# Kernel optimization log

Measured on AMD Instinct MI355X. Metric: run time of the kernel, lower is better.

Reference implementation:

```python
import jax, jax.numpy as jnp
import numpy as np

T, B, I, H = 512, 64, 512, 1024


def setup_inputs() -> dict:
    key = jax.random.key(0)
    ks = jax.random.split(key, 7)
    s = 0.03  # keep recurrent dynamics stable
    return {
        "X": jax.random.normal(ks[0], (T, B, I), jnp.float32),
        "h0": jax.random.normal(ks[1], (B, H), jnp.float32) * 0.1,
        "c0": jax.random.normal(ks[2], (B, H), jnp.float32) * 0.1,
        "Wi": jax.random.normal(ks[3], (4, I, H), jnp.float32) * s,
        "Wh": jax.random.normal(ks[4], (4, H, H), jnp.float32) * s,
        "bi": jnp.zeros((4, H), jnp.float32),
        "bh": jnp.zeros((4, H), jnp.float32),
    }


def reference(X, h0, c0, Wi, Wh, bi, bh):
    # Gate order along axis 0 of Wi/Wh/bi/bh: f, i, g, o (matches the torch module's
    # linear_if/hf, linear_ii/hi, linear_ig/hg, linear_io/ho pairs).
    b = bi + bh  # [4, H] combined bias, mathematically identical

    def step(carry, x_t):
        h, c = carry
        # z: [4, B, H] = x @ Wi_g + h @ Wh_g + b_g for each gate g
        z = (jnp.einsum('bi,gih->gbh', x_t, Wi)
             + jnp.einsum('bh,ghk->gbk', h, Wh)
             + b[:, None, :])
        f = jax.nn.sigmoid(z[0])
        i = jax.nn.sigmoid(z[1])
        g = jnp.tanh(z[2])
        o = jax.nn.sigmoid(z[3])
        c_new = f * c + i * g
        h_new = o * jnp.tanh(c_new)
        return (h_new, c_new), h_new

    (h_n, c_n), outputs = jax.lax.scan(step, (h0, c0), X)
    return outputs, h_n, c_n
```

## Files before the change

### kernel.cpp

```cpp
#include <hip/hip_runtime.h>
#include <stdint.h>

#define T_STEPS 512
#define NB 64
#define NI 512
#define NH 1024
#define NBLK 128

typedef __attribute__((ext_vector_type(8))) short short8;
typedef __attribute__((ext_vector_type(4))) float floatx4;
typedef __attribute__((ext_vector_type(16))) float floatx16;
typedef __attribute__((ext_vector_type(4))) unsigned short ushortx4;

__device__ __forceinline__ unsigned short f2bf(float f) {
  union { float f; uint32_t u; } v; v.f = f;
  return (unsigned short)((v.u + 0x7FFFu + ((v.u >> 16) & 1u)) >> 16);
}
__device__ __forceinline__ float bf2f(unsigned short s) {
  union { uint32_t u; float f; } v; v.u = ((uint32_t)s) << 16; return v.f;
}
__device__ __forceinline__ float sigmoid_f(float x) {
  return 1.0f / (1.0f + __expf(-x));
}
__device__ __forceinline__ float tanh_f(float x) {
  float xx = fminf(fmaxf(x, -15.0f), 15.0f);
  float e = __expf(2.0f * xx);
  return (e - 1.0f) / (e + 1.0f);
}


__global__ void convert_x(const float* __restrict__ X, unsigned short* __restrict__ Xb) {
  int i = blockIdx.x * 256 + threadIdx.x;
  floatx4 x = ((const floatx4*)X)[i];
  ushortx4 o;
  o[0] = f2bf(x[0]); o[1] = f2bf(x[1]); o[2] = f2bf(x[2]); o[3] = f2bf(x[3]);
  ((ushortx4*)Xb)[i] = o;
}

__global__ void transpose_bf16(const float* __restrict__ in, unsigned short* __restrict__ outp,
                               int K, int N) {
  __shared__ float tile[64][65];
  int g = blockIdx.z;
  int k0 = blockIdx.x * 64, n0 = blockIdx.y * 64;
  int tx = threadIdx.x & 63, ty = threadIdx.x >> 6;
  const float* src = in + (size_t)g * K * N;
  unsigned short* dst = outp + (size_t)g * K * N;
#pragma unroll
  for (int i = 0; i < 16; i++) {
    int r = ty * 16 + i;
    tile[r][tx] = src[(size_t)(k0 + r) * N + n0 + tx];
  }
  __syncthreads();
#pragma unroll
  for (int i = 0; i < 16; i++) {
    int r = ty * 16 + i;
    dst[(size_t)(n0 + r) * K + k0 + tx] = f2bf(tile[tx][r]);
  }
}

__global__ void prep_small(const float* __restrict__ bi, const float* __restrict__ bh,
                           const float* __restrict__ h0, float* __restrict__ bias,
                           unsigned short* __restrict__ hbuf0, unsigned* __restrict__ flags) {
  int i = blockIdx.x * 256 + threadIdx.x;
  if (i < NBLK) flags[i] = 0u;
  if (i < 4 * NH) bias[i] = bi[i] + bh[i];
  if (i < NB * NH) hbuf0[i] = f2bf(h0[i]);
}

__global__ __launch_bounds__(256) void gemm_zx(
    const unsigned short* __restrict__ Xb,
    const unsigned short* __restrict__ WibT,
    const float* __restrict__ bias,
    unsigned short* __restrict__ Zx) {
  __shared__ __align__(16) unsigned short As[128][40];
  __shared__ __align__(16) unsigned short Bs[128][40];
  const int g = blockIdx.z;
  const int m0 = blockIdx.x * 128;
  const int n0 = blockIdx.y * 128;
  const int tid = threadIdx.x;
  const int lane = tid & 63;
  const int wave = tid >> 6;
  const int wm = wave & 1, wn = wave >> 1;
  const int fr = lane & 15;
  const int fq = (lane >> 4) * 8;

  const unsigned short* Bsrc = WibT + (size_t)g * NH * NI;

  floatx4 acc[4][4];
#pragma unroll
  for (int a = 0; a < 4; a++)
#pragma unroll
    for (int b = 0; b < 4; b++)
#pragma unroll
      for (int z = 0; z < 4; z++) acc[a][b][z] = 0.0f;

  for (int k0 = 0; k0 < NI; k0 += 32) {
#pragma unroll
    for (int it = 0; it < 2; it++) {
      int c = tid + it * 256;
      int row = c >> 2, kc = (c & 3) * 8;
      *(uint4*)(&As[row][kc]) = *(const uint4*)(Xb + (size_t)(m0 + row) * NI + k0 + kc);
      *(uint4*)(&Bs[row][kc]) = *(const uint4*)(Bsrc + (size_t)(n0 + row) * NI + k0 + kc);
    }
    __syncthreads();
    short8 af[4], bf[4];
#pragma unroll
    for (int ms = 0; ms < 4; ms++) af[ms] = *(const short8*)(&As[wm * 64 + ms * 16 + fr][fq]);
#pragma unroll
    for (int ns = 0; ns < 4; ns++) bf[ns] = *(const short8*)(&Bs[wn * 64 + ns * 16 + fr][fq]);
#pragma unroll
    for (int ms = 0; ms < 4; ms++)
#pragma unroll
      for (int ns = 0; ns < 4; ns++)
        acc[ms][ns] = __builtin_amdgcn_mfma_f32_16x16x32_bf16(af[ms], bf[ns], acc[ms][ns], 0, 0, 0);
    __syncthreads();
  }

#pragma unroll
  for (int ns = 0; ns < 4; ns++) {
    int col = n0 + wn * 64 + ns * 16 + fr;
    float bs = bias[g * NH + col];
#pragma unroll
    for (int ms = 0; ms < 4; ms++) {
#pragma unroll
      for (int r = 0; r < 4; r++) {
        int m = m0 + wm * 64 + ms * 16 + (lane >> 4) * 4 + r;
        Zx[(size_t)m * 4096 + (size_t)g * NH + col] = f2bf(acc[ms][ns][r] + bs);
      }
    }
  }
}

__device__ __forceinline__ void issue_none() {}

template<int G>
__device__ __forceinline__ void load_a(const unsigned short* ap, short8 (&areg)[64]) {
  asm volatile("global_load_dwordx4 %0, %1, off offset:%2 sc0 sc1"
               : "=v"(areg[G]) : "v"(ap), "i"(G * 32));
}

template<int G>
__device__ __forceinline__ void load_b(const unsigned short* bfr, int lane, short8 (&bs)[64]) {
  bs[G] = *(const short8*)(&bfr[((size_t)(G * 64) + lane) * 8]);
}

template<int G>
struct Prolog {
  static __device__ __forceinline__ void run(const unsigned short* ap, short8 (&areg)[64]) {
    load_a<G>(ap, areg);
    Prolog<G + 1>::run(ap, areg);
  }
};
template<>
struct Prolog<16> {
  static __device__ __forceinline__ void run(const unsigned short*, short8 (&)[64]) {}
};

template<int G>
struct Chunks {
  static __device__ __forceinline__ void run(const unsigned short* ap, const unsigned short* bfr,
                                             int lane, short8 (&areg)[64], short8 (&bs)[64],
                                             floatx16& acc0, floatx16& acc1) {
    if constexpr (G + 16 < 64) load_a<G + 16>(ap, areg);
    if constexpr (G + 4 < 64) load_b<G + 4>(bfr, lane, bs);
    constexpr int NOUT = (G + 16 < 64) ? 16 : (63 - G);
    asm volatile("s_waitcnt vmcnt(%1)" : "+v"(areg[G]) : "i"(NOUT) : "memory");
    if constexpr ((G & 1) == 0)
      acc0 = __builtin_amdgcn_mfma_f32_32x32x16_bf16(areg[G], bs[G], acc0, 0, 0, 0);
    else
      acc1 = __builtin_amdgcn_mfma_f32_32x32x16_bf16(areg[G], bs[G], acc1, 0, 0, 0);
    Chunks<G + 1>::run(ap, bfr, lane, areg, bs, acc0, acc1);
  }
};
template<>
struct Chunks<64> {
  static __device__ __forceinline__ void run(const unsigned short*, const unsigned short*,
                                             int, short8 (&)[64], short8 (&)[64],
                                             floatx16&, floatx16&) {}
};

__global__ __launch_bounds__(128, 1) void lstm_persist(
    const unsigned short* __restrict__ Zx,
    const unsigned short* __restrict__ WhT,
    const float* __restrict__ c0,
    unsigned short* __restrict__ hbuf,
    unsigned* __restrict__ flags,
    float* __restrict__ out) {
  __shared__ __align__(16) unsigned short bfr[64 * 64 * 8];

  const int bk = blockIdx.x;
  const int j0 = bk * 8;
  const int tid = threadIdx.x;
  const int lane = tid & 63;
  const int wm = tid >> 6;
  const int nl = lane & 31;
  const int g0 = nl >> 3;
  const int jj = nl & 7;
  const int half = lane >> 5;

  for (int i = 0; i < 32; i++) {
    int f = tid + i * 128;
    int fl = f & 63, kk = f >> 6;
    int n = fl & 31;
    size_t wrow = (size_t)((n >> 3) * NH + j0 + (n & 7));
    int kb = kk * 16 + (fl >> 5) * 8;
    uint4 v = *(const uint4*)(WhT + wrow * NH + kb);
    *(uint4*)(&bfr[(size_t)f * 8]) = v;
  }

  float creg[16];
  int brow[16];
#pragma unroll
  for (int r = 0; r < 16; r++) {
    brow[r] = wm * 32 + (r & 3) + 8 * (r >> 2) + 4 * half;
    creg[r] = c0[(size_t)brow[r] * NH + j0 + jj];
  }
  __syncthreads();

  const int hsz = NB * NH;

  float zx[16];
  {
    const unsigned short* zbase = Zx + (size_t)g0 * NH + j0 + jj;
#pragma unroll
    for (int r = 0; r < 16; r++) zx[r] = bf2f(zbase[(size_t)brow[r] * 4096]);
  }

  for (int t = 0; t < T_STEPS; t++) {
    if (t) {
      unsigned tgt = (unsigned)t;
      for (;;) {
        unsigned a = __hip_atomic_load(flags + 2 * lane, __ATOMIC_RELAXED,
                                       __HIP_MEMORY_SCOPE_AGENT);
        unsigned b = __hip_atomic_load(flags + 2 * lane + 1, __ATOMIC_RELAXED,
                                       __HIP_MEMORY_SCOPE_AGENT);
        if (__all((int)(a >= tgt && b >= tgt))) break;
        __builtin_amdgcn_s_sleep(1);
      }
    }
    asm volatile("s_waitcnt vmcnt(0)" ::: "memory");
    __builtin_amdgcn_sched_barrier(0);

    const unsigned short* hin = hbuf + (size_t)(t & 1) * hsz;
    unsigned short* hout = hbuf + (size_t)((t + 1) & 1) * hsz;
    const unsigned short* ap = hin + (size_t)(wm * 32 + nl) * NH + half * 8;

    floatx16 acc0, acc1;
#pragma unroll
    for (int z = 0; z < 16; z++) { acc0[z] = 0.0f; acc1[z] = 0.0f; }

    short8 areg[64];
    short8 bs[64];
    Prolog<0>::run(ap, areg);
    load_b<0>(bfr, lane, bs);
    load_b<1>(bfr, lane, bs);
    load_b<2>(bfr, lane, bs);
    load_b<3>(bfr, lane, bs);
    Chunks<0>::run(ap, bfr, lane, areg, bs, acc0, acc1);
    __builtin_amdgcn_sched_barrier(0);

#pragma unroll
    for (int z = 0; z < 16; z++) acc0[z] += acc1[z];

#pragma unroll
    for (int r = 0; r < 16; r++) {
      float z0 = acc0[r] + zx[r];
      float z1 = __shfl_xor(z0, 8);
      float z2 = __shfl_xor(z0, 16);
      float z3 = __shfl_xor(z1, 16);
      bool bb0 = (g0 & 1) != 0, bb1 = (g0 & 2) != 0;
      float zf = bb1 ? (bb0 ? z3 : z2) : (bb0 ? z1 : z0);
      float zi = bb1 ? (bb0 ? z2 : z3) : (bb0 ? z0 : z1);
      float zg = bb1 ? (bb0 ? z1 : z0) : (bb0 ? z3 : z2);
      float zo = bb1 ? (bb0 ? z0 : z1) : (bb0 ? z2 : z3);
      float fg = sigmoid_f(zf);
      float ig = sigmoid_f(zi);
      float gg = tanh_f(zg);
      float og = sigmoid_f(zo);
      float c = fg * creg[r] + ig * gg;
      creg[r] = c;
      float h = og * tanh_f(c);
      if (g0 == 0) {
        size_t oidx = (size_t)brow[r] * NH + j0 + jj;
        out[(size_t)t * hsz + oidx] = h;
        __hip_atomic_store(&hout[oidx], f2bf(h), __ATOMIC_RELAXED,
                           __HIP_MEMORY_SCOPE_AGENT);
        if (t == T_STEPS - 1) out[(size_t)T_STEPS * hsz + oidx] = h;
      }
    }

    if (t + 1 < T_STEPS) {
      asm volatile("s_waitcnt vmcnt(0)" ::: "memory");
      __syncthreads();
      if (tid == 0)
        __hip_atomic_store(flags + bk, (unsigned)(t + 1),
                           __ATOMIC_RELAXED, __HIP_MEMORY_SCOPE_AGENT);
      const unsigned short* zbase =
          Zx + (size_t)(t + 1) * (NB * 4096) + (size_t)g0 * NH + j0 + jj;
#pragma unroll
      for (int r = 0; r < 16; r++) zx[r] = bf2f(zbase[(size_t)brow[r] * 4096]);
    }
  }

  if (g0 == 0) {
#pragma unroll
    for (int r = 0; r < 16; r++)
      out[(size_t)T_STEPS * NB * NH + NB * NH + (size_t)brow[r] * NH + j0 + jj] = creg[r];
  }
}

extern "C" void kernel_launch(void* const* d_in, const int* in_sizes, int n_in,
                              void* d_out, int out_size, void* d_ws, size_t ws_size,
                              hipStream_t stream) {
  const float* X  = (const float*)d_in[0];
  const float* h0 = (const float*)d_in[1];
  const float* c0 = (const float*)d_in[2];
  const float* Wi = (const float*)d_in[3];
  const float* Wh = (const float*)d_in[4];
  const float* bi = (const float*)d_in[5];
  const float* bh = (const float*)d_in[6];
  float* out = (float*)d_out;

  uint8_t* ws = (uint8_t*)d_ws;
  size_t off = 0;
  auto alloc = [&](size_t bytes) -> void* {
    void* p = ws + off;
    off += (bytes + 255) & ~(size_t)255;
    return p;
  };
  unsigned short* Zx   = (unsigned short*)alloc((size_t)T_STEPS * NB * 4096 * 2);
  unsigned short* Xb   = (unsigned short*)alloc((size_t)T_STEPS * NB * NI * 2);
  unsigned short* WibT = (unsigned short*)alloc((size_t)4 * NH * NI * 2);
  unsigned short* WhT  = (unsigned short*)alloc((size_t)4 * NH * NH * 2);
  float* bias          = (float*)alloc((size_t)4 * NH * 4);
  unsigned short* hbuf = (unsigned short*)alloc((size_t)2 * NB * NH * 2);
  unsigned* flags      = (unsigned*)alloc((size_t)NBLK * 32 * 4);

  if (off > ws_size) {
    hipMemsetAsync(d_out, 0x7F, (size_t)out_size * 4, stream);
    return;
  }

  convert_x<<<16384, 256, 0, stream>>>(X, Xb);
  transpose_bf16<<<dim3(8, 16, 4), 256, 0, stream>>>(Wi, WibT, NI, NH);
  transpose_bf16<<<dim3(16, 16, 4), 256, 0, stream>>>(Wh, WhT, NH, NH);
  prep_small<<<256, 256, 0, stream>>>(bi, bh, h0, bias, hbuf, flags);
  gemm_zx<<<dim3(256, 8, 4), 256, 0, stream>>>(Xb, WibT, bias, Zx);

  lstm_persist<<<dim3(NBLK), dim3(128), 0, stream>>>(Zx, WhT, c0, hbuf, flags, out);
}
```

Before: 5.807 ms.

## Repack Zx into per-block contiguous layout and prefetch it across the step

The input-projection GEMM now writes its bf16 results, staged through shared memory, in a layout where each persistent block's per-step gate slice is contiguous. The recurrent kernel can then fetch its 16 Zx values with two 16-byte non-temporal loads, issued right after the MFMA chain and double-buffered across a two-step unrolled loop, where it previously used 16 scattered scalar loads after the flag publish. The flag poll becomes one 64-bit load instead of two 32-bit loads, and the h output stores are moved after the flag release and made non-temporal, taking them off the critical path. The risks are extra shared memory in the GEMM, higher register pressure from the prefetch buffers, and a more complex index mapping.

Measured after the change: 6.048 ms. 4.1% more time.

```diff
diff --git a/kernel.cpp b/kernel.cpp
--- a/kernel.cpp
+++ b/kernel.cpp
@@ -71,9 +71,10 @@
     const unsigned short* __restrict__ Xb,
     const unsigned short* __restrict__ WibT,
     const float* __restrict__ bias,
-    unsigned short* __restrict__ Zx) {
+    unsigned short* __restrict__ Zq) {
   __shared__ __align__(16) unsigned short As[128][40];
   __shared__ __align__(16) unsigned short Bs[128][40];
+  __shared__ __align__(16) unsigned short stg[16384];
   const int g = blockIdx.z;
   const int m0 = blockIdx.x * 128;
   const int n0 = blockIdx.y * 128;
@@ -118,20 +119,37 @@
 
 #pragma unroll
   for (int ns = 0; ns < 4; ns++) {
-    int col = n0 + wn * 64 + ns * 16 + fr;
-    float bs = bias[g * NH + col];
+    int jrel = wn * 64 + ns * 16 + fr;
+    float bs = bias[g * NH + n0 + jrel];
+    int bkp = jrel >> 3, jj = jrel & 7;
 #pragma unroll
     for (int ms = 0; ms < 4; ms++) {
 #pragma unroll
       for (int r = 0; r < 4; r++) {
-        int m = m0 + wm * 64 + ms * 16 + (lane >> 4) * 4 + r;
-        Zx[(size_t)m * 4096 + (size_t)g * NH + col] = f2bf(acc[ms][ns][r] + bs);
+        int mrel = wm * 64 + ms * 16 + (lane >> 4) * 4 + r;
+        int tp = mrel >> 6, b = mrel & 63;
+        int wm2 = b >> 5, row32 = b & 31;
+        int half2 = (row32 >> 2) & 1;
+        int rr = (row32 & 3) | ((row32 >> 3) << 2);
+        int idx = (((((tp * 16 + bkp) * 2 + wm2) * 2 + half2) * 8 + jj) * 16) + rr;
+        stg[idx] = f2bf(acc[ms][ns][r] + bs);
       }
     }
   }
-}
-
-__device__ __forceinline__ void issue_none() {}
+  __syncthreads();
+  const size_t t0 = (size_t)(m0 >> 6);
+  const int bk0 = n0 >> 3;
+#pragma unroll
+  for (int tp = 0; tp < 2; tp++) {
+    size_t gbase = (((t0 + tp) * 4 + g) * 128 + bk0) * 512;
+#pragma unroll
+    for (int c = 0; c < 4; c++) {
+      int e = c * 2048 + tid * 8;
+      *(uint4*)(Zq + gbase + e) = *(const uint4*)(stg + tp * 8192 + e);
+    }
+  }
+}
+
 
 template<int G>
 __device__ __forceinline__ void load_a(const unsigned short* ap, short8 (&areg)[64]) {
@@ -179,8 +197,108 @@
                                              floatx16&, floatx16&) {}
 };
 
+__device__ __forceinline__ void lstm_step(
+    int t, const unsigned short* __restrict__ Zq, unsigned short* __restrict__ hbuf,
+    unsigned* __restrict__ flags, float* __restrict__ out,
+    const unsigned short* bfr, const unsigned long long* fpq,
+    int tid, int lane, int wm, int nl, int g0, int jj, int half, int bk, int j0,
+    size_t zoff, const int (&brow)[16], float (&creg)[16],
+    uint4 (&zc)[2], uint4 (&zn)[2]) {
+  const int hsz = NB * NH;
+
+  if (t) {
+    unsigned tgt = (unsigned)t;
+    for (;;) {
+      unsigned long long fv = __hip_atomic_load(fpq, __ATOMIC_RELAXED,
+                                                __HIP_MEMORY_SCOPE_AGENT);
+      unsigned a = (unsigned)fv, b2 = (unsigned)(fv >> 32);
+      if (__all((int)((a >= tgt) && (b2 >= tgt)))) break;
+      __builtin_amdgcn_s_sleep(1);
+    }
+  }
+  asm volatile("s_waitcnt vmcnt(0)" ::: "memory");
+  __builtin_amdgcn_sched_barrier(0);
+
+  const unsigned short* hin = hbuf + (size_t)(t & 1) * hsz;
+  unsigned short* hout = hbuf + (size_t)((t + 1) & 1) * hsz;
+  const unsigned short* ap = hin + (size_t)(wm * 32 + nl) * NH + half * 8;
+
+  floatx16 acc0, acc1;
+#pragma unroll
+  for (int z = 0; z < 16; z++) { acc0[z] = 0.0f; acc1[z] = 0.0f; }
+
+  short8 areg[64];
+  short8 bs[64];
+  Prolog<0>::run(ap, areg);
+  load_b<0>(bfr, lane, bs);
+  load_b<1>(bfr, lane, bs);
+  load_b<2>(bfr, lane, bs);
+  load_b<3>(bfr, lane, bs);
+  Chunks<0>::run(ap, bfr, lane, areg, bs, acc0, acc1);
+  __builtin_amdgcn_sched_barrier(0);
+
+  if (t + 1 < T_STEPS) {
+    const unsigned short* zp = Zq + (size_t)(t + 1) * 262144 + zoff;
+    asm volatile("global_load_dwordx4 %0, %1, off nt" : "=v"(zn[0]) : "v"(zp));
+    asm volatile("global_load_dwordx4 %0, %1, off offset:16 nt" : "=v"(zn[1]) : "v"(zp));
+  }
+
+#pragma unroll
+  for (int z = 0; z < 16; z++) acc0[z] += acc1[z];
+
+  unsigned zd[8];
+  zd[0] = zc[0].x; zd[1] = zc[0].y; zd[2] = zc[0].z; zd[3] = zc[0].w;
+  zd[4] = zc[1].x; zd[5] = zc[1].y; zd[6] = zc[1].z; zd[7] = zc[1].w;
+
+  float harr[16];
+#pragma unroll
+  for (int r = 0; r < 16; r++) {
+    unsigned dw = zd[r >> 1];
+    float zxv = bf2f((unsigned short)((r & 1) ? (dw >> 16) : (dw & 0xffffu)));
+    float z0 = acc0[r] + zxv;
+    float z1 = __shfl_xor(z0, 8);
+    float z2 = __shfl_xor(z0, 16);
+    float z3 = __shfl_xor(z1, 16);
+    bool bb0 = (g0 & 1) != 0, bb1 = (g0 & 2) != 0;
+    float zf = bb1 ? (bb0 ? z3 : z2) : (bb0 ? z1 : z0);
+    float zi = bb1 ? (bb0 ? z2 : z3) : (bb0 ? z0 : z1);
+    float zg = bb1 ? (bb0 ? z1 : z0) : (bb0 ? z3 : z2);
+    float zo = bb1 ? (bb0 ? z0 : z1) : (bb0 ? z2 : z3);
+    float fg = sigmoid_f(zf);
+    float ig = sigmoid_f(zi);
+    float gg = tanh_f(zg);
+    float og = sigmoid_f(zo);
+    float c = fg * creg[r] + ig * gg;
+    creg[r] = c;
+    float h = og * tanh_f(c);
+    harr[r] = h;
+    if (g0 == 0) {
+      __hip_atomic_store(&hout[(size_t)brow[r] * NH + j0 + jj], f2bf(h),
+                         __ATOMIC_RELAXED, __HIP_MEMORY_SCOPE_AGENT);
+    }
+  }
+
+  if (t + 1 < T_STEPS) {
+    asm volatile("s_waitcnt vmcnt(0)" ::: "memory");
+    __syncthreads();
+    if (tid == 0)
+      __hip_atomic_store(flags + bk, (unsigned)(t + 1),
+                         __ATOMIC_RELAXED, __HIP_MEMORY_SCOPE_AGENT);
+  }
+
+  if (g0 == 0) {
+#pragma unroll
+    for (int r = 0; r < 16; r++) {
+      size_t oidx = (size_t)brow[r] * NH + j0 + jj;
+      __builtin_nontemporal_store(harr[r], &out[(size_t)t * hsz + oidx]);
+      if (t == T_STEPS - 1)
+        __builtin_nontemporal_store(harr[r], &out[(size_t)T_STEPS * hsz + oidx]);
+    }
+  }
+}
+
 __global__ __launch_bounds__(128, 1) void lstm_persist(
-    const unsigned short* __restrict__ Zx,
+    const unsigned short* __restrict__ Zq,
     const unsigned short* __restrict__ WhT,
     const float* __restrict__ c0,
     unsigned short* __restrict__ hbuf,
@@ -217,95 +335,28 @@
   }
   __syncthreads();
 
-  const int hsz = NB * NH;
-
-  float zx[16];
+  const unsigned long long* fpq = (const unsigned long long*)flags + lane;
+  const size_t zoff = (((((size_t)g0 * 128 + bk) * 2 + wm) * 2 + half) * 8 + jj) * 16;
+
+  uint4 zA[2], zB[2];
   {
-    const unsigned short* zbase = Zx + (size_t)g0 * NH + j0 + jj;
-#pragma unroll
-    for (int r = 0; r < 16; r++) zx[r] = bf2f(zbase[(size_t)brow[r] * 4096]);
-  }
-
-  for (int t = 0; t < T_STEPS; t++) {
-    if (t) {
-      unsigned tgt = (unsigned)t;
-      for (;;) {
-        unsigned a = __hip_atomic_load(flags + 2 * lane, __ATOMIC_RELAXED,
-                                       __HIP_MEMORY_SCOPE_AGENT);
-        unsigned b = __hip_atomic_load(flags + 2 * lane + 1, __ATOMIC_RELAXED,
-                                       __HIP_MEMORY_SCOPE_AGENT);
-        if (__all((int)(a >= tgt && b >= tgt))) break;
-        __builtin_amdgcn_s_sleep(1);
-      }
-    }
-    asm volatile("s_waitcnt vmcnt(0)" ::: "memory");
-    __builtin_amdgcn_sched_barrier(0);
-
-    const unsigned short* hin = hbuf + (size_t)(t & 1) * hsz;
-    unsigned short* hout = hbuf + (size_t)((t + 1) & 1) * hsz;
-    const unsigned short* ap = hin + (size_t)(wm * 32 + nl) * NH + half * 8;
-
-    floatx16 acc0, acc1;
-#pragma unroll
-    for (int z = 0; z < 16; z++) { acc0[z] = 0.0f; acc1[z] = 0.0f; }
-
-    short8 areg[64];
-    short8 bs[64];
-    Prolog<0>::run(ap, areg);
-    load_b<0>(bfr, lane, bs);
-    load_b<1>(bfr, lane, bs);
-    load_b<2>(bfr, lane, bs);
-    load_b<3>(bfr, lane, bs);
-    Chunks<0>::run(ap, bfr, lane, areg, bs, acc0, acc1);
-    __builtin_amdgcn_sched_barrier(0);
-
-#pragma unroll
-    for (int z = 0; z < 16; z++) acc0[z] += acc1[z];
-
-#pragma unroll
-    for (int r = 0; r < 16; r++) {
-      float z0 = acc0[r] + zx[r];
-      float z1 = __shfl_xor(z0, 8);
-      float z2 = __shfl_xor(z0, 16);
-      float z3 = __shfl_xor(z1, 16);
-      bool bb0 = (g0 & 1) != 0, bb1 = (g0 & 2) != 0;
-      float zf = bb1 ? (bb0 ? z3 : z2) : (bb0 ? z1 : z0);
-      float zi = bb1 ? (bb0 ? z2 : z3) : (bb0 ? z0 : z1);
-      float zg = bb1 ? (bb0 ? z1 : z0) : (bb0 ? z3 : z2);
-      float zo = bb1 ? (bb0 ? z0 : z1) : (bb0 ? z2 : z3);
-      float fg = sigmoid_f(zf);
-      float ig = sigmoid_f(zi);
-      float gg = tanh_f(zg);
-      float og = sigmoid_f(zo);
-      float c = fg * creg[r] + ig * gg;
-      creg[r] = c;
-      float h = og * tanh_f(c);
-      if (g0 == 0) {
-        size_t oidx = (size_t)brow[r] * NH + j0 + jj;
-        out[(size_t)t * hsz + oidx] = h;
-        __hip_atomic_store(&hout[oidx], f2bf(h), __ATOMIC_RELAXED,
-                           __HIP_MEMORY_SCOPE_AGENT);
-        if (t == T_STEPS - 1) out[(size_t)T_STEPS * hsz + oidx] = h;
-      }
-    }
-
-    if (t + 1 < T_STEPS) {
-      asm volatile("s_waitcnt vmcnt(0)" ::: "memory");
-      __syncthreads();
-      if (tid == 0)
-        __hip_atomic_store(flags + bk, (unsigned)(t + 1),
-                           __ATOMIC_RELAXED, __HIP_MEMORY_SCOPE_AGENT);
-      const unsigned short* zbase =
-          Zx + (size_t)(t + 1) * (NB * 4096) + (size_t)g0 * NH + j0 + jj;
-#pragma unroll
-      for (int r = 0; r < 16; r++) zx[r] = bf2f(zbase[(size_t)brow[r] * 4096]);
-    }
+    const unsigned short* zp = Zq + zoff;
+    asm volatile("global_load_dwordx4 %0, %1, off nt" : "=v"(zA[0]) : "v"(zp));
+    asm volatile("global_load_dwordx4 %0, %1, off offset:16 nt" : "=v"(zA[1]) : "v"(zp));
+  }
+
+  for (int t2 = 0; t2 < T_STEPS; t2 += 2) {
+    lstm_step(t2,     Zq, hbuf, flags, out, bfr, fpq, tid, lane, wm, nl, g0, jj, half,
+              bk, j0, zoff, brow, creg, zA, zB);
+    lstm_step(t2 + 1, Zq, hbuf, flags, out, bfr, fpq, tid, lane, wm, nl, g0, jj, half,
+              bk, j0, zoff, brow, creg, zB, zA);
   }
 
   if (g0 == 0) {
 #pragma unroll
     for (int r = 0; r < 16; r++)
-      out[(size_t)T_STEPS * NB * NH + NB * NH + (size_t)brow[r] * NH + j0 + jj] = creg[r];
+      __builtin_nontemporal_store(
+          creg[r], &out[(size_t)T_STEPS * NB * NH + NB * NH + (size_t)brow[r] * NH + j0 + jj]);
   }
 }
 
@@ -328,7 +379,7 @@
     off += (bytes + 255) & ~(size_t)255;
     return p;
   };
-  unsigned short* Zx   = (unsigned short*)alloc((size_t)T_STEPS * NB * 4096 * 2);
+  unsigned short* Zq   = (unsigned short*)alloc((size_t)T_STEPS * NB * 4096 * 2);
   unsigned short* Xb   = (unsigned short*)alloc((size_t)T_STEPS * NB * NI * 2);
   unsigned short* WibT = (unsigned short*)alloc((size_t)4 * NH * NI * 2);
   unsigned short* WhT  = (unsigned short*)alloc((size_t)4 * NH * NH * 2);
@@ -345,7 +396,7 @@
   transpose_bf16<<<dim3(8, 16, 4), 256, 0, stream>>>(Wi, WibT, NI, NH);
   transpose_bf16<<<dim3(16, 16, 4), 256, 0, stream>>>(Wh, WhT, NH, NH);
   prep_small<<<256, 256, 0, stream>>>(bi, bh, h0, bias, hbuf, flags);
-  gemm_zx<<<dim3(256, 8, 4), 256, 0, stream>>>(Xb, WibT, bias, Zx);
-
-  lstm_persist<<<dim3(NBLK), dim3(128), 0, stream>>>(Zx, WhT, c0, hbuf, flags, out);
-}
+  gemm_zx<<<dim3(256, 8, 4), 256, 0, stream>>>(Xb, WibT, bias, Zq);
+
+  lstm_persist<<<dim3(NBLK), dim3(128), 0, stream>>>(Zq, WhT, c0, hbuf, flags, out);
+}
```
